# Performance work log

Hardware: AMD Instinct MI355X
Metric: run time of the kernel (lower is better)

The kernel has to match this reference:

```python
import jax, jax.numpy as jnp
import numpy as np

T, B, I, H = 2048, 64, 256, 256


def setup_inputs() -> dict:
    key = jax.random.key(0)
    k_x, k_w, k_hh = jax.random.split(key, 3)
    x = jax.random.normal(k_x, (T, B, I), dtype=jnp.float32)
    # input-to-hidden weight for the 3 gates [r, z, n], torch GRU layout [3H, I]
    W_ih = jax.random.normal(k_w, (3 * H, I), dtype=jnp.float32) * (1.0 / np.sqrt(H))
    # biases are zero-filled in IndGRU.__init__ but remain parameters
    b_ih = jnp.zeros((3 * H,), dtype=jnp.float32)
    b_hh = jnp.zeros((3 * H,), dtype=jnp.float32)
    # per-unit (diagonal) recurrent weights, uniform(-1, 1), rows = [r, z, n]
    w_hh = jax.random.uniform(k_hh, (3, H), dtype=jnp.float32, minval=-1.0, maxval=1.0)
    return {"x": x, "W_ih": W_ih, "b_ih": b_ih, "b_hh": b_hh, "w_hh": w_hh}


def reference(x, W_ih, b_ih, b_hh, w_hh):
    # x: [T, B, I] time-major (torch GRU default). Diagonal-recurrence GRU:
    # the hidden-to-hidden matmul collapses to an elementwise multiply per gate.
    Bsz = x.shape[1]
    Hsz = w_hh.shape[1]
    # Precompute all input-side gate pre-activations in one big GEMM: [T, B, 3H]
    gx = jnp.einsum('tbi,gi->tbg', x, W_ih) + b_ih
    gxr, gxz, gxn = jnp.split(gx, 3, axis=-1)
    w_hr, w_hz, w_hn = w_hh[0], w_hh[1], w_hh[2]
    b_hr, b_hz, b_hn = jnp.split(b_hh, 3)

    def step(h, g):
        xr, xz, xn = g
        r = jax.nn.sigmoid(xr + w_hr * h + b_hr)
        z = jax.nn.sigmoid(xz + w_hz * h + b_hz)
        n = jnp.tanh(xn + r * (w_hn * h + b_hn))
        h_new = (1.0 - z) * n + z * h
        return h_new, h_new

    h0 = jnp.zeros((Bsz, Hsz), dtype=x.dtype)
    h_n, out = jax.lax.scan(step, h0, (gxr, gxz, gxn))
    # torch GRU returns (output [T,B,H], h_n [num_layers=1, B, H])
    return out, h_n[None]
```

## Files before the change

kernel.cpp:

```cpp
#include <hip/hip_runtime.h>
#include <stdint.h>

#define T_LEN 2048
#define BATCH 64
#define I_DIM 256
#define H_DIM 256
#define N3    768
#define M_ROWS (T_LEN*BATCH)
#define L2E 1.4426950408889634f

typedef _Float16 f16;
typedef __attribute__((ext_vector_type(4))) float  f32x4;
typedef __attribute__((ext_vector_type(4))) _Float16 f16x4;
typedef __attribute__((ext_vector_type(8))) _Float16 f16x8;

__global__ void convert_w(const float* __restrict__ W, f16* __restrict__ Whf) {
    int idx = blockIdx.x * 256 + threadIdx.x;
    int r = idx >> 8, c = idx & 255;
    float scale = (r < 2*H_DIM) ? -L2E : -2.0f*L2E;
    int chunk = c >> 5, lu = (c >> 3) & 3, e = c & 7;
    int pu = (lu + (r >> 1)) & 3;
    Whf[r*256 + chunk*32 + pu*8 + e] = (f16)(W[idx] * scale);
}

#define BM 256
#define BN 128
#define BK 32

__global__ __launch_bounds__(512, 4) void gemm_gx(
        const float* __restrict__ X,
        const f16* __restrict__ Whf,
        f16* __restrict__ gxP) {
    __shared__ union {
        struct { f16 A[BM*BK]; f16 B[2][BN*BK]; } s;
        f16 C[64*128*4];
    } u;

    int wg   = blockIdx.x;
    int orig = (wg & 7) * 384 + (wg >> 3);
    int mblk = orig / 6, nblk = orig - mblk * 6;
    int m0 = mblk * BM, n0 = nblk * BN;

    int tid = threadIdx.x, lane = tid & 63, wid = tid >> 6;
    int wm = wid >> 1, wn = wid & 1;
    int arow = tid >> 3, acol = tid & 7;

    f32x4 acc[4][4] = {};

    auto issueB = [&](int kb, int buf) {
        int lrow = wid * 16 + (lane >> 2);
        const f16* g = Whf + (size_t)(n0 + lrow) * 256 + kb * 32 + (lane & 3) * 8;
        f16* l = &u.s.B[buf][wid * 16 * BK];
        __builtin_amdgcn_global_load_lds(
            (const __attribute__((address_space(1))) void*)g,
            (__attribute__((address_space(3))) void*)l, 16, 0, 0);
    };

    issueB(0, 0);
    int cur = 0;
    for (int kb = 0; kb < 8; ++kb) {
        f32x4 ra[4];
        #pragma unroll
        for (int p = 0; p < 4; ++p)
            ra[p] = *(const f32x4*)(X + (size_t)(m0 + p*64 + arow) * I_DIM + kb*BK + acol*4);
        __syncthreads();
        #pragma unroll
        for (int p = 0; p < 4; ++p) {
            int row = p*64 + arow;
            f16x4 hv;
            #pragma unroll
            for (int e = 0; e < 4; ++e) hv[e] = (f16)ra[p][e];
            int pu = ((acol >> 1) + (row >> 1)) & 3;
            *(f16x4*)((char*)u.s.A + row*64 + pu*16 + (acol & 1)*8) = hv;
        }
        __syncthreads();
        if (kb < 7) issueB(kb + 1, cur ^ 1);
        f16x8 af[4], bf[4];
        #pragma unroll
        for (int mi = 0; mi < 4; ++mi) {
            int lrow = wm*64 + mi*16 + (lane & 15);
            int pu = ((lane >> 4) + (lrow >> 1)) & 3;
            af[mi] = *(const f16x8*)((const char*)u.s.A + lrow*64 + pu*16);
        }
        #pragma unroll
        for (int ni = 0; ni < 4; ++ni) {
            int lrow = wn*64 + ni*16 + (lane & 15);
            int pu = ((lane >> 4) + (lrow >> 1)) & 3;
            bf[ni] = *(const f16x8*)((const char*)u.s.B[cur] + lrow*64 + pu*16);
        }
        #pragma unroll
        for (int mi = 0; mi < 4; ++mi)
          #pragma unroll
          for (int ni = 0; ni < 4; ++ni)
            acc[mi][ni] = __builtin_amdgcn_mfma_f32_16x16x32_f16(af[mi], bf[ni], acc[mi][ni], 0,0,0);
        cur ^= 1;
    }

    __syncthreads();
    #pragma unroll
    for (int mi = 0; mi < 4; ++mi) {
        int bb0 = mi*16 + (lane >> 4)*4;
        #pragma unroll
        for (int ni = 0; ni < 4; ++ni) {
            int c = wn*64 + ni*16 + (lane & 15);
            #pragma unroll
            for (int j = 0; j < 4; ++j)
                u.C[(bb0 + j)*512 + c*4 + wm] = (f16)acc[mi][ni][j];
        }
    }
    __syncthreads();
    #pragma unroll
    for (int i = 0; i < 8; ++i) {
        int idx = i*512 + tid, bb = idx >> 6, w = idx & 63;
        f16x8 v = *(const f16x8*)&u.C[bb*512 + w*8];
        *(f16x8*)(gxP + ((size_t)(mblk*64 + bb)*N3 + n0)*4 + w*8) = v;
    }
}

__global__ __launch_bounds__(64) void indgru_scan(
        const f16* __restrict__ gxP, const float* __restrict__ bih,
        const float* __restrict__ bhh, const float* __restrict__ whh,
        float* __restrict__ out) {
    int lane = threadIdx.x;
    int b = blockIdx.x >> 2;
    int h = (blockIdx.x & 3) * 64 + lane;

    float whr = -L2E  * whh[h];
    float whz = -L2E  * whh[H_DIM + h];
    float whn = -2.0f*L2E * whh[2*H_DIM + h];
    float cr  = -L2E  * (bih[h] + bhh[h]);
    float cz  = -L2E  * (bih[H_DIM+h] + bhh[H_DIM+h]);
    float cn  = -2.0f*L2E * bih[2*H_DIM+h];
    float bhn = -2.0f*L2E * bhh[2*H_DIM+h];

    const size_t stb = (size_t)BATCH * N3 * 4;
    const size_t so  = (size_t)BATCH * H_DIM;
    const f16* pr = gxP + ((size_t)b * N3 + h) * 4;
    float* po = out + (size_t)b * H_DIM + h;

    f16x4 Ar[4], Az[4], An[4], Br[4], Bz[4], Bn[4];
    float hv = 0.f;

#define LOADG(R, Z, N, grp) do {                                    \
        const f16* _p = pr + (size_t)(grp) * 4 * stb;               \
        _Pragma("unroll")                                           \
        for (int _q = 0; _q < 4; ++_q) {                            \
            R[_q] = *(const f16x4*)(_p);                            \
            Z[_q] = *(const f16x4*)(_p + H_DIM*4);                  \
            N[_q] = *(const f16x4*)(_p + 2*H_DIM*4);                \
            _p += stb;                                              \
        }                                                           \
    } while (0)

#define PROC16(R, Z, N) do {                                        \
        _Pragma("unroll")                                           \
        for (int _q = 0; _q < 4; ++_q)                              \
        _Pragma("unroll")                                           \
        for (int _j = 0; _j < 4; ++_j) {                            \
            float ur = (float)R[_q][_j] + cr;                       \
            float uz = (float)Z[_q][_j] + cz;                       \
            float un = (float)N[_q][_j] + cn;                       \
            float er = __builtin_amdgcn_exp2f(fmaf(whr, hv, ur));   \
            float r  = __builtin_amdgcn_rcpf(1.f + er);             \
            float ez = __builtin_amdgcn_exp2f(fmaf(whz, hv, uz));   \
            float z  = __builtin_amdgcn_rcpf(1.f + ez);             \
            float mn = fmaf(whn, hv, bhn);                          \
            float en = __builtin_amdgcn_exp2f(fmaf(r, mn, un));     \
            float q  = __builtin_amdgcn_rcpf(1.f + en);             \
            float hp1 = hv + 1.f;                                   \
            hv = fmaf(z, fmaf(-2.f, q, hp1), fmaf(2.f, q, -1.f));   \
            *po = hv; po += so;                                     \
        }                                                           \
    } while (0)

    LOADG(Ar, Az, An, 0);
    for (int i = 0; i < 63; ++i) {
        LOADG(Br, Bz, Bn, 2*i + 1);
        PROC16(Ar, Az, An);
        LOADG(Ar, Az, An, 2*i + 2);
        PROC16(Br, Bz, Bn);
    }
    LOADG(Br, Bz, Bn, 127);
    PROC16(Ar, Az, An);
    PROC16(Br, Bz, Bn);

    out[(size_t)T_LEN * so + (size_t)b * H_DIM + h] = hv;
#undef LOADG
#undef PROC16
}

extern "C" void kernel_launch(void* const* d_in, const int* in_sizes, int n_in,
                              void* d_out, int out_size, void* d_ws, size_t ws_size,
                              hipStream_t stream) {
    const float* x   = (const float*)d_in[0];
    const float* Wih = (const float*)d_in[1];
    const float* bih = (const float*)d_in[2];
    const float* bhh = (const float*)d_in[3];
    const float* whh = (const float*)d_in[4];
    float* out = (float*)d_out;

    char* ws = (char*)d_ws;
    f16* gxP = (f16*)ws;
    f16* Whf = (f16*)(ws + (size_t)M_ROWS * N3 * sizeof(f16));

    convert_w<<<(N3*I_DIM)/256, 256, 0, stream>>>(Wih, Whf);
    gemm_gx<<<(M_ROWS/BM)*(N3/BN), 512, 0, stream>>>(x, Whf, gxP);
    indgru_scan<<<BATCH*(H_DIM/64), 64, 0, stream>>>(gxP, bih, bhh, whh, out);
}
```

Measured before the change: 518.0 us.

## Pre-convert X to fp16 in a separate pass and stream both GEMM operands via LDS DMA

```diff
diff --git a/kernel.cpp b/kernel.cpp
--- a/kernel.cpp
+++ b/kernel.cpp
@@ -11,109 +11,120 @@
 
 typedef _Float16 f16;
 typedef __attribute__((ext_vector_type(4))) float  f32x4;
-typedef __attribute__((ext_vector_type(4))) _Float16 f16x4;
+typedef __attribute__((ext_vector_type(2))) _Float16 f16x2;
 typedef __attribute__((ext_vector_type(8))) _Float16 f16x8;
 
-__global__ void convert_w(const float* __restrict__ W, f16* __restrict__ Whf) {
-    int idx = blockIdx.x * 256 + threadIdx.x;
-    int r = idx >> 8, c = idx & 255;
-    float scale = (r < 2*H_DIM) ? -L2E : -2.0f*L2E;
-    int chunk = c >> 5, lu = (c >> 3) & 3, e = c & 7;
-    int pu = (lu + (r >> 1)) & 3;
-    Whf[r*256 + chunk*32 + pu*8 + e] = (f16)(W[idx] * scale);
-}
-
-#define BM 256
-#define BN 128
-#define BK 32
-
-__global__ __launch_bounds__(512, 4) void gemm_gx(
-        const float* __restrict__ X,
-        const f16* __restrict__ Whf,
+__global__ __launch_bounds__(256) void convert_x(const float* __restrict__ X,
+                                                 f16* __restrict__ Xs) {
+    const int U = M_ROWS * 32;
+    for (int u = blockIdx.x * 256 + threadIdx.x; u < U; u += 2048 * 256) {
+        int m = u >> 5, gu = u & 31;
+        int su = (gu & 24) | ((gu & 7) ^ (m & 7));
+        const float* src = X + (size_t)m * 256 + su * 8;
+        f32x4 a = *(const f32x4*)src;
+        f32x4 b = *(const f32x4*)(src + 4);
+        f16x8 v;
+        #pragma unroll
+        for (int e = 0; e < 4; ++e) { v[e] = (f16)a[e]; v[4+e] = (f16)b[e]; }
+        *(f16x8*)(Xs + (size_t)m * 256 + gu * 8) = v;
+    }
+}
+
+__global__ __launch_bounds__(256) void convert_w(const float* __restrict__ W,
+                                                 f16* __restrict__ Ws) {
+    int u = blockIdx.x * 256 + threadIdx.x;
+    int n = u >> 5, gu = u & 31;
+    float scale = (n < 512) ? -L2E : -2.0f * L2E;
+    int su = (gu & 24) | ((gu & 7) ^ (n & 7));
+    const float* src = W + (size_t)n * 256 + su * 8;
+    f32x4 a = *(const f32x4*)src;
+    f32x4 b = *(const f32x4*)(src + 4);
+    f16x8 v;
+    #pragma unroll
+    for (int e = 0; e < 4; ++e) { v[e] = (f16)(a[e]*scale); v[4+e] = (f16)(b[e]*scale); }
+    *(f16x8*)(Ws + (size_t)n * 256 + gu * 8) = v;
+}
+
+__global__ __launch_bounds__(256, 4) void gemm_gx(
+        const f16* __restrict__ Xs,
+        const f16* __restrict__ Ws,
         f16* __restrict__ gxP) {
     __shared__ union {
-        struct { f16 A[BM*BK]; f16 B[2][BN*BK]; } s;
-        f16 C[64*128*4];
+        struct { f16 A[128*64]; f16 B[128*64]; } s;
+        f16 C[64*128*2];
     } u;
 
     int wg   = blockIdx.x;
-    int orig = (wg & 7) * 384 + (wg >> 3);
+    int orig = (wg & 7) * 768 + (wg >> 3);
     int mblk = orig / 6, nblk = orig - mblk * 6;
-    int m0 = mblk * BM, n0 = nblk * BN;
+    int m0 = mblk * 128, n0 = nblk * 128;
 
     int tid = threadIdx.x, lane = tid & 63, wid = tid >> 6;
     int wm = wid >> 1, wn = wid & 1;
-    int arow = tid >> 3, acol = tid & 7;
 
     f32x4 acc[4][4] = {};
 
-    auto issueB = [&](int kb, int buf) {
-        int lrow = wid * 16 + (lane >> 2);
-        const f16* g = Whf + (size_t)(n0 + lrow) * 256 + kb * 32 + (lane & 3) * 8;
-        f16* l = &u.s.B[buf][wid * 16 * BK];
-        __builtin_amdgcn_global_load_lds(
-            (const __attribute__((address_space(1))) void*)g,
-            (__attribute__((address_space(3))) void*)l, 16, 0, 0);
-    };
-
-    issueB(0, 0);
-    int cur = 0;
-    for (int kb = 0; kb < 8; ++kb) {
-        f32x4 ra[4];
-        #pragma unroll
-        for (int p = 0; p < 4; ++p)
-            ra[p] = *(const f32x4*)(X + (size_t)(m0 + p*64 + arow) * I_DIM + kb*BK + acol*4);
+    for (int kb = 0; kb < 4; ++kb) {
+        if (kb) __syncthreads();
+        #pragma unroll
+        for (int rd = 0; rd < 4; ++rd) {
+            int uu = rd * 256 + tid;
+            int row = uu >> 3, pl = uu & 7;
+            const f16* ga = Xs + (size_t)(m0 + row) * 256 + kb * 64 + pl * 8;
+            __builtin_amdgcn_global_load_lds(
+                (const __attribute__((address_space(1))) void*)ga,
+                (__attribute__((address_space(3))) void*)(u.s.A + uu * 8), 16, 0, 0);
+        }
+        #pragma unroll
+        for (int rd = 0; rd < 4; ++rd) {
+            int uu = rd * 256 + tid;
+            int row = uu >> 3, pl = uu & 7;
+            const f16* gb = Ws + (size_t)(n0 + row) * 256 + kb * 64 + pl * 8;
+            __builtin_amdgcn_global_load_lds(
+                (const __attribute__((address_space(1))) void*)gb,
+                (__attribute__((address_space(3))) void*)(u.s.B + uu * 8), 16, 0, 0);
+        }
         __syncthreads();
         #pragma unroll
-        for (int p = 0; p < 4; ++p) {
-            int row = p*64 + arow;
-            f16x4 hv;
-            #pragma unroll
-            for (int e = 0; e < 4; ++e) hv[e] = (f16)ra[p][e];
-            int pu = ((acol >> 1) + (row >> 1)) & 3;
-            *(f16x4*)((char*)u.s.A + row*64 + pu*16 + (acol & 1)*8) = hv;
-        }
-        __syncthreads();
-        if (kb < 7) issueB(kb + 1, cur ^ 1);
-        f16x8 af[4], bf[4];
-        #pragma unroll
-        for (int mi = 0; mi < 4; ++mi) {
-            int lrow = wm*64 + mi*16 + (lane & 15);
-            int pu = ((lane >> 4) + (lrow >> 1)) & 3;
-            af[mi] = *(const f16x8*)((const char*)u.s.A + lrow*64 + pu*16);
-        }
-        #pragma unroll
-        for (int ni = 0; ni < 4; ++ni) {
-            int lrow = wn*64 + ni*16 + (lane & 15);
-            int pu = ((lane >> 4) + (lrow >> 1)) & 3;
-            bf[ni] = *(const f16x8*)((const char*)u.s.B[cur] + lrow*64 + pu*16);
-        }
-        #pragma unroll
-        for (int mi = 0; mi < 4; ++mi)
-          #pragma unroll
-          for (int ni = 0; ni < 4; ++ni)
-            acc[mi][ni] = __builtin_amdgcn_mfma_f32_16x16x32_f16(af[mi], bf[ni], acc[mi][ni], 0,0,0);
-        cur ^= 1;
+        for (int kk = 0; kk < 2; ++kk) {
+            int c16 = kk * 4 + (lane >> 4);
+            f16x8 af[4], bf[4];
+            #pragma unroll
+            for (int mi = 0; mi < 4; ++mi) {
+                int row = wm*64 + mi*16 + (lane & 15);
+                af[mi] = *(const f16x8*)((const char*)u.s.A + row*128 + ((c16 ^ (row & 7)) * 16));
+            }
+            #pragma unroll
+            for (int ni = 0; ni < 4; ++ni) {
+                int row = wn*64 + ni*16 + (lane & 15);
+                bf[ni] = *(const f16x8*)((const char*)u.s.B + row*128 + ((c16 ^ (row & 7)) * 16));
+            }
+            #pragma unroll
+            for (int mi = 0; mi < 4; ++mi)
+              #pragma unroll
+              for (int ni = 0; ni < 4; ++ni)
+                acc[mi][ni] = __builtin_amdgcn_mfma_f32_16x16x32_f16(af[mi], bf[ni], acc[mi][ni], 0,0,0);
+        }
     }
 
     __syncthreads();
     #pragma unroll
     for (int mi = 0; mi < 4; ++mi) {
-        int bb0 = mi*16 + (lane >> 4)*4;
+        int rr = mi*16 + (lane >> 4)*4;
         #pragma unroll
         for (int ni = 0; ni < 4; ++ni) {
             int c = wn*64 + ni*16 + (lane & 15);
             #pragma unroll
             for (int j = 0; j < 4; ++j)
-                u.C[(bb0 + j)*512 + c*4 + wm] = (f16)acc[mi][ni][j];
+                u.C[(rr + j)*256 + c*2 + wm] = (f16)acc[mi][ni][j];
         }
     }
     __syncthreads();
     #pragma unroll
     for (int i = 0; i < 8; ++i) {
-        int idx = i*512 + tid, bb = idx >> 6, w = idx & 63;
-        f16x8 v = *(const f16x8*)&u.C[bb*512 + w*8];
-        *(f16x8*)(gxP + ((size_t)(mblk*64 + bb)*N3 + n0)*4 + w*8) = v;
+        int uu = i*256 + tid, b = uu >> 5, q = uu & 31;
+        f16x8 v = *(const f16x8*)(u.C + b*256 + q*8);
+        *(f16x8*)(gxP + (size_t)(mblk*64 + b)*1536 + n0*2 + q*8) = v;
     }
 }
 
@@ -133,30 +144,30 @@
     float cn  = -2.0f*L2E * bih[2*H_DIM+h];
     float bhn = -2.0f*L2E * bhh[2*H_DIM+h];
 
-    const size_t stb = (size_t)BATCH * N3 * 4;
+    const size_t stp = (size_t)BATCH * N3 * 2;
     const size_t so  = (size_t)BATCH * H_DIM;
-    const f16* pr = gxP + ((size_t)b * N3 + h) * 4;
+    const f16* pr = gxP + (size_t)b * 1536 + h * 2;
     float* po = out + (size_t)b * H_DIM + h;
 
-    f16x4 Ar[4], Az[4], An[4], Br[4], Bz[4], Bn[4];
+    f16x2 Ar[8], Az[8], An[8], Br[8], Bz[8], Bn[8];
     float hv = 0.f;
 
 #define LOADG(R, Z, N, grp) do {                                    \
-        const f16* _p = pr + (size_t)(grp) * 4 * stb;               \
+        const f16* _p = pr + (size_t)(grp) * 8 * stp;               \
         _Pragma("unroll")                                           \
-        for (int _q = 0; _q < 4; ++_q) {                            \
-            R[_q] = *(const f16x4*)(_p);                            \
-            Z[_q] = *(const f16x4*)(_p + H_DIM*4);                  \
-            N[_q] = *(const f16x4*)(_p + 2*H_DIM*4);                \
-            _p += stb;                                              \
+        for (int _q = 0; _q < 8; ++_q) {                            \
+            R[_q] = *(const f16x2*)(_p);                            \
+            Z[_q] = *(const f16x2*)(_p + 512);                      \
+            N[_q] = *(const f16x2*)(_p + 1024);                     \
+            _p += stp;                                              \
         }                                                           \
     } while (0)
 
 #define PROC16(R, Z, N) do {                                        \
         _Pragma("unroll")                                           \
-        for (int _q = 0; _q < 4; ++_q)                              \
+        for (int _q = 0; _q < 8; ++_q)                              \
         _Pragma("unroll")                                           \
-        for (int _j = 0; _j < 4; ++_j) {                            \
+        for (int _j = 0; _j < 2; ++_j) {                            \
             float ur = (float)R[_q][_j] + cr;                       \
             float uz = (float)Z[_q][_j] + cz;                       \
             float un = (float)N[_q][_j] + cn;                       \
@@ -201,9 +212,11 @@
 
     char* ws = (char*)d_ws;
     f16* gxP = (f16*)ws;
-    f16* Whf = (f16*)(ws + (size_t)M_ROWS * N3 * sizeof(f16));
-
-    convert_w<<<(N3*I_DIM)/256, 256, 0, stream>>>(Wih, Whf);
-    gemm_gx<<<(M_ROWS/BM)*(N3/BN), 512, 0, stream>>>(x, Whf, gxP);
+    f16* Xs  = (f16*)(ws + (size_t)M_ROWS*N3*sizeof(f16));
+    f16* Wsc = Xs + (size_t)M_ROWS*I_DIM;
+
+    convert_x<<<2048, 256, 0, stream>>>(x, Xs);
+    convert_w<<<(N3*I_DIM/8)/256, 256, 0, stream>>>(Wih, Wsc);
+    gemm_gx<<<(M_ROWS/128)*(N3/128), 256, 0, stream>>>(Xs, Wsc, gxP);
     indgru_scan<<<BATCH*(H_DIM/64), 64, 0, stream>>>(gxP, bih, bhh, whh, out);
 }
```

Result: faster. 499.9 us (-3.5%).
